# Optimization experiments

Measured on AMD Instinct MI355X. Metric: run time of the kernel, lower is better.

The kernel has to match this reference:

```python
import jax, jax.numpy as jnp
import numpy as np

B, N, DIM, QK, H, GS = 4, 4096, 512, 512, 8, 128
NUM_LABELS = 8
R_BASE, R_MIN, R_MAX = 0.5, 0.25, 0.75
LAMBDA_P, LAMBDA_V, CCR = 0.25, 0.25, 0.125


def setup_inputs() -> dict:
    key = jax.random.key(0)
    ks = jax.random.split(key, 7)
    s = DIM ** -0.5
    return {
        "x": jax.random.normal(ks[0], (B, N, DIM), jnp.float32),
        "labels": jax.random.randint(ks[1], (B, N), 0, NUM_LABELS),
        "scores": jax.random.uniform(ks[2], (B, N), jnp.float32),
        "Wq": jax.random.normal(ks[3], (DIM, QK), jnp.float32) * s,
        "Wk": jax.random.normal(ks[4], (DIM, QK), jnp.float32) * s,
        "Wv": jax.random.normal(ks[5], (DIM, DIM), jnp.float32) * s,
        "Wproj": jax.random.normal(ks[6], (DIM, DIM), jnp.float32) * s,
    }


def _windows(t, gs, ng):
    # pad with flipped last-group tail, then overlapping windows of size 2*gs, stride gs
    tp = jnp.concatenate([t, jnp.flip(t[:, -gs:], axis=1)], axis=1)
    a = tp.reshape(t.shape[0], ng + 1, gs, *t.shape[2:])
    return jnp.concatenate([a[:, :-1], a[:, 1:]], axis=2)  # [b, ng, 2*gs, ...]


def _topk_mask(vals, keep, cand):
    # rank of each entry when sorted descending; keep top-`keep` among candidates
    ranks = jnp.argsort(jnp.argsort(-vals, axis=-1), axis=-1)
    return (ranks < keep[:, :, None, None, None]) & cand


def reference(x, labels, scores, Wq, Wk, Wv, Wproj):
    b, n, _ = x.shape
    gs = GS
    ng = n // gs            # num_tokens divisible by group_size -> pad_n = 0
    ws = 2 * gs
    q = x @ Wq
    k = x @ Wk
    v = x @ Wv

    qw = q.reshape(b, ng, gs, H, -1).transpose(0, 1, 3, 2, 4)          # b ng h gs d
    kw = _windows(k, gs, ng).reshape(b, ng, ws, H, -1).transpose(0, 1, 3, 2, 4)
    vw = _windows(v, gs, ng).reshape(b, ng, ws, H, -1).transpose(0, 1, 3, 2, 4)
    q_labels = labels.reshape(b, ng, gs)
    k_labels = _windows(labels, gs, ng)                                 # b ng ws
    q_scores = scores.reshape(b, ng, gs)
    k_scores = _windows(scores, gs, ng)

    d = qw.shape[-1]
    scale = 1.0 / jnp.sqrt(jnp.asarray(d, qw.dtype))
    logits = jnp.einsum('bghqd,bghkd->bghqk', qw, kw) * scale           # b ng h gs ws
    attn_hat = jax.nn.softmax(logits, axis=-1)  # no prev_attn_state -> attn_hat = attn_cur

    # dynamic focus ratio: purity from group mode label + score variance
    counts = jax.nn.one_hot(q_labels, NUM_LABELS, dtype=jnp.float32).sum(axis=2)  # b ng L
    mode = jnp.argmax(counts, axis=-1)
    purity = jnp.mean((q_labels == mode[..., None]).astype(jnp.float32), axis=-1)
    score_var = jnp.var(q_scores.astype(jnp.float32), axis=-1)  # unbiased=False
    focus = jnp.clip(R_BASE + LAMBDA_P * purity - LAMBDA_V * score_var, R_MIN, R_MAX)

    keep = jnp.clip(jnp.ceil(focus * ws).astype(jnp.int32), 1, ws)
    cross_keep = jnp.round(keep.astype(jnp.float32) * CCR).astype(jnp.int32)
    cross_keep = jnp.where(keep > 1, jnp.maximum(cross_keep, 1), 0)
    same_keep = jnp.maximum(keep - cross_keep, 1)

    same_mask = (q_labels[:, :, None, :, None] == k_labels[:, :, None, None, :])  # b ng 1 gs ws

    same_scores = jnp.where(same_mask, attn_hat, -10000.0)
    m_same = _topk_mask(same_scores, same_keep, same_mask)
    pair_conf = q_scores[:, :, None, :, None] * k_scores[:, :, None, None, :]
    cross_scores = attn_hat * pair_conf
    m_cross = _topk_mask(cross_scores, cross_keep, ~same_mask)
    final_mask = m_same | m_cross

    sparse_logits = jnp.where(final_mask, logits, -10000.0)
    attn_local = jax.nn.softmax(sparse_logits, axis=-1)
    attn_local = jnp.where(final_mask, attn_local, 0.0)
    attn_local = attn_local / (attn_local.sum(axis=-1, keepdims=True) + 1e-9)

    out = jnp.einsum('bghqk,bghkd->bghqd', attn_local, vw)
    out = out.transpose(0, 1, 3, 2, 4).reshape(b, ng * gs, -1)[:, :n]
    return out @ Wproj, attn_local
```

## Files before the change

kernel.cpp:

```cpp
#include <hip/hip_runtime.h>

#define BB 4
#define NN 4096
#define DIMM 512
#define HH 8
#define DH 64
#define GSZ 128
#define NGRP 32
#define WSZ 256
#define CHUNK 32

#define MK 8388608u
#define WK 262144u

typedef short short8 __attribute__((ext_vector_type(8)));
typedef float f32x4 __attribute__((ext_vector_type(4)));

__device__ inline unsigned short bf16rne(float f) {
  unsigned u = __float_as_uint(f);
  unsigned r = u + 0x7FFFu + ((u >> 16) & 1u);
  return (unsigned short)(r >> 16);
}
__device__ inline float bf16tof(unsigned short h) {
  return __uint_as_float(((unsigned)h) << 16);
}

__global__ __launch_bounds__(256) void split_planes(
    const float* __restrict__ X, unsigned short* __restrict__ P)
{
  unsigned idx = (blockIdx.x * 256u + threadIdx.x) * 4u;
  float4 xv = *(const float4*)&X[idx];
  float xs[4] = {xv.x, xv.y, xv.z, xv.w};
  ushort4 hv, mv, lv;
  unsigned short* hp = (unsigned short*)&hv;
  unsigned short* mp = (unsigned short*)&mv;
  unsigned short* lp = (unsigned short*)&lv;
#pragma unroll
  for (int i = 0; i < 4; ++i) {
    unsigned short h = bf16rne(xs[i]);
    float r1 = xs[i] - bf16tof(h);
    unsigned short m = bf16rne(r1);
    float r2 = r1 - bf16tof(m);
    hp[i] = h;
    mp[i] = m;
    lp[i] = bf16rne(r2);
  }
  *(ushort4*)&P[idx] = hv;
  *(ushort4*)&P[MK + idx] = mv;
  *(ushort4*)&P[2u * MK + idx] = lv;
}

__global__ __launch_bounds__(256) void split_w(
    const float* __restrict__ Wq, const float* __restrict__ Wk,
    const float* __restrict__ Wv, const float* __restrict__ Wpj,
    unsigned short* __restrict__ wqkv, unsigned short* __restrict__ wproj)
{
  unsigned e = blockIdx.x * 256u + threadIdx.x;
  int mz = e >> 18;
  unsigned rem = e & (WK - 1u);
  unsigned kk = rem >> 9, n = rem & 511u;
  const float* src = (mz == 0) ? Wq : (mz == 1) ? Wk : (mz == 2) ? Wv : Wpj;
  float w = src[kk * 512u + n];
  unsigned short h = bf16rne(w);
  float r1 = w - bf16tof(h);
  unsigned short m = bf16rne(r1);
  float r2 = r1 - bf16tof(m);
  unsigned short l = bf16rne(r2);
  unsigned o = n * 512u + kk;
  if (mz < 3) {
    unsigned short* base = wqkv + (unsigned)mz * 3u * WK;
    base[o] = h;
    base[WK + o] = m;
    base[2u * WK + o] = l;
  } else {
    wproj[o] = h;
    wproj[WK + o] = m;
  }
}

template <int NP, int NT>
__global__ __launch_bounds__(256) void mfma_gemm(
    const unsigned short* __restrict__ Ap,
    const unsigned short* __restrict__ Wp,
    float* __restrict__ C)
{
  constexpr int ta[6] = {0, 0, 1, 1, 0, 2};
  constexpr int tw[6] = {0, 1, 0, 1, 2, 0};
  const int z = blockIdx.z;
  const int n0 = blockIdx.x * 128;
  const int m0 = blockIdx.y * 128;
  const int tid = threadIdx.x;
  const int lane = tid & 63, wv = tid >> 6;
  const int wm = (wv >> 1) * 64, wn = (wv & 1) * 64;
  const int lm = lane & 15, lk = (lane >> 4) * 8;

  __shared__ unsigned short As[NP * 128 * 40];
  __shared__ unsigned short Ws[NP * 128 * 40];

  f32x4 acc[4][4];
#pragma unroll
  for (int i = 0; i < 4; ++i)
#pragma unroll
    for (int j = 0; j < 4; ++j) acc[i][j] = (f32x4){0.f, 0.f, 0.f, 0.f};

  const unsigned short* Wz = Wp + (size_t)z * NP * WK;

  for (int k0 = 0; k0 < 512; k0 += 32) {
#pragma unroll
    for (int i = 0; i < NP * 2; ++i) {
      int idx = i * 256 + tid;
      int p = idx >> 9, rem = idx & 511;
      int r = rem >> 2, cc = rem & 3;
      *(short8*)&As[p * 5120 + r * 40 + cc * 8] =
          *(const short8*)&Ap[(size_t)p * MK + (size_t)(m0 + r) * 512 + k0 + cc * 8];
      *(short8*)&Ws[p * 5120 + r * 40 + cc * 8] =
          *(const short8*)&Wz[(size_t)p * WK + (size_t)(n0 + r) * 512 + k0 + cc * 8];
    }
    __syncthreads();

    short8 a[NP][4];
#pragma unroll
    for (int p = 0; p < NP; ++p)
#pragma unroll
      for (int fm = 0; fm < 4; ++fm)
        a[p][fm] = *(const short8*)&As[p * 5120 + (wm + fm * 16 + lm) * 40 + lk];

#pragma unroll
    for (int fn = 0; fn < 4; ++fn) {
      short8 bf[NP];
#pragma unroll
      for (int p = 0; p < NP; ++p)
        bf[p] = *(const short8*)&Ws[p * 5120 + (wn + fn * 16 + lm) * 40 + lk];
#pragma unroll
      for (int fm = 0; fm < 4; ++fm) {
#pragma unroll
        for (int t = 0; t < NT; ++t)
          acc[fm][fn] = __builtin_amdgcn_mfma_f32_16x16x32_bf16(
              a[ta[t]][fm], bf[tw[t]], acc[fm][fn], 0, 0, 0);
      }
    }
    __syncthreads();
  }

  const int rq = (lane >> 4) * 4;
  float* Cz = C + (size_t)z * 8388608u;
#pragma unroll
  for (int fm = 0; fm < 4; ++fm)
#pragma unroll
    for (int fn = 0; fn < 4; ++fn) {
      int row = m0 + wm + fm * 16 + rq;
      int col = n0 + wn + fn * 16 + lm;
#pragma unroll
      for (int r = 0; r < 4; ++r)
        Cz[(size_t)(row + r) * 512 + col] = acc[fm][fn][r];
    }
}

__global__ __launch_bounds__(256) void gemm512(
    const float* __restrict__ A,
    const float* __restrict__ W0, const float* __restrict__ W1, const float* __restrict__ W2,
    float* __restrict__ C0, float* __restrict__ C1, float* __restrict__ C2)
{
  const int z = blockIdx.z;
  const float* Wm = (z == 0) ? W0 : (z == 1 ? W1 : W2);
  float* Cm = (z == 0) ? C0 : (z == 1 ? C1 : C2);
  const int n0 = blockIdx.x * 128;
  const int m0 = blockIdx.y * 128;
  const int tid = threadIdx.x;
  const int tx = tid & 15, ty = tid >> 4;

  __shared__ float As[32][132];
  __shared__ float Bs[32][132];

  float acc[8][8];
#pragma unroll
  for (int i = 0; i < 8; ++i)
#pragma unroll
    for (int j = 0; j < 8; ++j) acc[i][j] = 0.f;

  for (int k0 = 0; k0 < 512; k0 += 32) {
    {
      const int c4 = tid & 7, r = tid >> 3;
#pragma unroll
      for (int p = 0; p < 128; p += 32) {
        float4 av = *(const float4*)&A[(size_t)(m0 + r + p) * 512 + k0 + c4 * 4];
        As[c4 * 4 + 0][r + p] = av.x;
        As[c4 * 4 + 1][r + p] = av.y;
        As[c4 * 4 + 2][r + p] = av.z;
        As[c4 * 4 + 3][r + p] = av.w;
      }
      const int j4 = tid & 31, rb = tid >> 5;
#pragma unroll
      for (int p = 0; p < 32; p += 8) {
        *(float4*)&Bs[rb + p][j4 * 4] =
            *(const float4*)&Wm[(size_t)(k0 + rb + p) * 512 + n0 + j4 * 4];
      }
    }
    __syncthreads();
#pragma unroll
    for (int kk = 0; kk < 32; ++kk) {
      float4 a0 = *(const float4*)&As[kk][ty * 8];
      float4 a1 = *(const float4*)&As[kk][ty * 8 + 4];
      float4 b0 = *(const float4*)&Bs[kk][tx * 8];
      float4 b1 = *(const float4*)&Bs[kk][tx * 8 + 4];
      float av[8] = {a0.x, a0.y, a0.z, a0.w, a1.x, a1.y, a1.z, a1.w};
      float bv[8] = {b0.x, b0.y, b0.z, b0.w, b1.x, b1.y, b1.z, b1.w};
#pragma unroll
      for (int i = 0; i < 8; ++i)
#pragma unroll
        for (int j = 0; j < 8; ++j) acc[i][j] += av[i] * bv[j];
    }
    __syncthreads();
  }
#pragma unroll
  for (int i = 0; i < 8; ++i) {
    size_t row = (size_t)(m0 + ty * 8 + i);
    float4 o0 = make_float4(acc[i][0], acc[i][1], acc[i][2], acc[i][3]);
    float4 o1 = make_float4(acc[i][4], acc[i][5], acc[i][6], acc[i][7]);
    *(float4*)&Cm[row * 512 + n0 + tx * 8] = o0;
    *(float4*)&Cm[row * 512 + n0 + tx * 8 + 4] = o1;
  }
}

__device__ __forceinline__ void focus_keep(
    const unsigned char* klab, const float* kscr, int* hist8, float* s_var,
    int* s_sk, int* s_ck, int tid, int lane, int wv)
{
  if (tid < GSZ) atomicAdd(&hist8[klab[tid]], 1);
  if (wv == 0) {
    double x0 = (double)kscr[lane], x1 = (double)kscr[lane + 64];
    double s = x0 + x1;
#pragma unroll
    for (int off = 32; off > 0; off >>= 1) s += __shfl_xor(s, off);
    double mean = s * (1.0 / 128.0);
    double d0 = x0 - mean, d1 = x1 - mean;
    double vs = d0 * d0 + d1 * d1;
#pragma unroll
    for (int off = 32; off > 0; off >>= 1) vs += __shfl_xor(vs, off);
    if (lane == 0) *s_var = (float)(vs * (1.0 / 128.0));
  }
  __syncthreads();
  if (tid == 0) {
    int bc = hist8[0];
    for (int l = 1; l < 8; ++l)
      if (hist8[l] > bc) bc = hist8[l];
    float purity = (float)bc * (1.0f / GSZ);
    float focus = 0.5f + 0.25f * purity - 0.25f * (*s_var);
    focus = fminf(fmaxf(focus, 0.25f), 0.75f);
    int keep = (int)ceilf(focus * (float)WSZ);
    keep = min(max(keep, 1), WSZ);
    int ck = keep >> 3, rem = keep & 7;
    if (rem > 4 || (rem == 4 && (ck & 1))) ck++;
    if (ck < 1) ck = 1;
    int sk = keep - ck;
    if (sk < 1) sk = 1;
    *s_sk = sk;
    *s_ck = ck;
  }
  __syncthreads();
}

__global__ __launch_bounds__(256, 3) void attn_v9(
    const float* __restrict__ q, const float* __restrict__ k,
    const float* __restrict__ vf,
    const int* __restrict__ labels, const float* __restrict__ scores,
    float* __restrict__ attn_out, unsigned short* __restrict__ opl)
{
  const int bx = blockIdx.x;
  const int c = bx >> 10;
  const int rblk = bx & 1023;
  const int h = rblk & 7;
  const int g = (rblk >> 3) & 31;
  const int b = rblk >> 8;
  const int r0 = c * CHUNK;
  const int tid = threadIdx.x;
  const int lane = tid & 63, wv = tid >> 6;
  const int lm = lane & 15, lq = lane >> 4;

  __shared__ float att[CHUNK][264];
  __shared__ __align__(16) unsigned char vbuf[18432];
  float (*ktile)[68] = (float (*)[68])vbuf;
  unsigned short* vtT = (unsigned short*)vbuf;
  __shared__ unsigned char klab[WSZ];
  __shared__ float kscr[WSZ];
  __shared__ int hist8[8];
  __shared__ float s_var;
  __shared__ int s_sk, s_ck;

  {
    int j = tid;
    int pos = g * GSZ + j;
    int tok = pos < NN ? pos : (2 * NN - 1 - pos);
    klab[j] = (unsigned char)labels[b * NN + tok];
    kscr[j] = scores[b * NN + tok];
  }
  if (tid < 8) hist8[tid] = 0;
  __syncthreads();
  focus_keep(klab, kscr, hist8, &s_var, &s_sk, &s_ck, tid, lane, wv);
  const int same_keep = s_sk, cross_keep = s_ck;

  const int rp = tid >> 4, jx = tid & 15;
  const int srow = tid >> 4, sd4 = (tid & 15) * 4;
  const float* q0p = q + (size_t)(b * NN + g * GSZ + r0 + rp) * DIMM + h * DH;
  const float* q1p = q0p + (size_t)16 * DIMM;

  for (int jt = 0; jt < 4; ++jt) {
#pragma unroll
    for (int p = 0; p < 64; p += 16) {
      int j = jt * 64 + srow + p;
      int pos = g * GSZ + j;
      int tok = pos < NN ? pos : (2 * NN - 1 - pos);
      *(float4*)&ktile[srow + p][sd4] =
          *(const float4*)&k[(size_t)(b * NN + tok) * DIMM + h * DH + sd4];
    }
    __syncthreads();
    float acc0[4] = {0.f, 0.f, 0.f, 0.f}, acc1[4] = {0.f, 0.f, 0.f, 0.f};
#pragma unroll
    for (int dd = 0; dd < DH; dd += 4) {
      float4 q0 = *(const float4*)(q0p + dd);
      float4 q1 = *(const float4*)(q1p + dd);
#pragma unroll
      for (int jj = 0; jj < 4; ++jj) {
        float4 kv = *(const float4*)&ktile[jx + 16 * jj][dd];
        acc0[jj] += q0.x * kv.x + q0.y * kv.y + q0.z * kv.z + q0.w * kv.w;
        acc1[jj] += q1.x * kv.x + q1.y * kv.y + q1.z * kv.z + q1.w * kv.w;
      }
    }
#pragma unroll
    for (int jj = 0; jj < 4; ++jj) {
      att[rp][jt * 64 + jx + 16 * jj] = acc0[jj] * 0.125f;
      att[rp + 16][jt * 64 + jx + 16 * jj] = acc1[jj] * 0.125f;
    }
    __syncthreads();
  }

  {
    int kl0[4];
    float ks0[4];
#pragma unroll
    for (int m = 0; m < 4; ++m) {
      kl0[m] = klab[lane + 64 * m];
      ks0[m] = kscr[lane + 64 * m];
    }
    for (int sp = 0; sp < 4; ++sp) {
      const int rA = wv * 8 + 2 * sp, rB = rA + 1;
      const int qLA = klab[r0 + rA], qLB = klab[r0 + rB];
      const float qSA = kscr[r0 + rA], qSB = kscr[r0 + rB];
      float aA[4], aB[4];
      float mxA = -INFINITY, mxB = -INFINITY;
#pragma unroll
      for (int m = 0; m < 4; ++m) {
        aA[m] = att[rA][lane + 64 * m];
        aB[m] = att[rB][lane + 64 * m];
        mxA = fmaxf(mxA, aA[m]);
        mxB = fmaxf(mxB, aB[m]);
      }
#pragma unroll
      for (int off = 32; off > 0; off >>= 1) {
        mxA = fmaxf(mxA, __shfl_xor(mxA, off));
        mxB = fmaxf(mxB, __shfl_xor(mxB, off));
      }
      unsigned fsA[4], fcA[4], fsB[4], fcB[4];
      bool cdA[4], cdB[4];
#pragma unroll
      for (int m = 0; m < 4; ++m) {
        aA[m] = expf(aA[m] - mxA);
        aB[m] = expf(aB[m] - mxB);
        cdA[m] = (kl0[m] == qLA);
        cdB[m] = (kl0[m] == qLB);
        fsA[m] = cdA[m] ? __float_as_uint(aA[m]) : 0u;
        fsB[m] = cdB[m] ? __float_as_uint(aB[m]) : 0u;
        fcA[m] = __float_as_uint(aA[m] * (qSA * ks0[m]));
        fcB[m] = __float_as_uint(aB[m] * (qSB * ks0[m]));
      }
      unsigned tsA = 0, tcA = 0, tsB = 0, tcB = 0;
      for (int bit = 29; bit >= 0; --bit) {
        unsigned csA = tsA | (1u << bit), ccA = tcA | (1u << bit);
        unsigned csB = tsB | (1u << bit), ccB = tcB | (1u << bit);
        int nsA = 0, ncA = 0, nsB = 0, ncB = 0;
#pragma unroll
        for (int m = 0; m < 4; ++m) {
          nsA += __popcll(__ballot(fsA[m] >= csA));
          ncA += __popcll(__ballot(fcA[m] >= ccA));
          nsB += __popcll(__ballot(fsB[m] >= csB));
          ncB += __popcll(__ballot(fcB[m] >= ccB));
        }
        if (nsA >= same_keep) tsA = csA;
        if (ncA >= cross_keep) tcA = ccA;
        if (nsB >= same_keep) tsB = csB;
        if (ncB >= cross_keep) tcB = ccB;
      }
#pragma unroll
      for (int rsel = 0; rsel < 2; ++rsel) {
        const int rr = rsel ? rB : rA;
        const unsigned ts = rsel ? tsB : tsA, tc = rsel ? tcB : tcA;
        unsigned* fs = rsel ? fsB : fsA;
        unsigned* fc = rsel ? fcB : fcA;
        float* a = rsel ? aB : aA;
        bool* cand = rsel ? cdB : cdA;
        unsigned long long beqs[4], beqc[4];
        int gts = 0, gtc = 0;
#pragma unroll
        for (int m = 0; m < 4; ++m) {
          gts += __popcll(__ballot(fs[m] > ts));
          gtc += __popcll(__ballot(fc[m] > tc));
          beqs[m] = __ballot(fs[m] == ts);
          beqc[m] = __ballot(fc[m] == tc);
        }
        const int rs = same_keep - gts, rc = cross_keep - gtc;
        float pv[4];
        float S = 0.f;
        int pres = 0, prec = 0;
#pragma unroll
        for (int m = 0; m < 4; ++m) {
          int mbs = __builtin_amdgcn_mbcnt_hi((unsigned)(beqs[m] >> 32),
                     __builtin_amdgcn_mbcnt_lo((unsigned)beqs[m], 0));
          int mbc = __builtin_amdgcn_mbcnt_hi((unsigned)(beqc[m] >> 32),
                     __builtin_amdgcn_mbcnt_lo((unsigned)beqc[m], 0));
          bool keep_s = cand[m] && ((fs[m] > ts) || ((fs[m] == ts) && (pres + mbs < rs)));
          bool keep_c = (!cand[m]) && ((fc[m] > tc) || ((fc[m] == tc) && (prec + mbc < rc)));
          pv[m] = (keep_s || keep_c) ? a[m] : 0.f;
          S += pv[m];
          pres += __popcll(beqs[m]);
          prec += __popcll(beqc[m]);
        }
#pragma unroll
        for (int off = 32; off > 0; off >>= 1) S += __shfl_xor(S, off);
        const float inv = 1.0f / S;
        size_t gb = ((((size_t)b * NGRP + g) * HH + h) * GSZ + (r0 + rr)) * WSZ + lane;
        unsigned short* prow = (unsigned short*)&att[rr][0];
#pragma unroll
        for (int m = 0; m < 4; ++m) {
          float p = pv[m] * inv;
          attn_out[gb + 64 * m] = p;
          unsigned short hh = bf16rne(p);
          prow[lane + 64 * m] = hh;
          prow[264 + lane + 64 * m] = bf16rne(p - bf16tof(hh));
        }
      }
    }
  }

  f32x4 acc2[2] = {(f32x4){0.f, 0.f, 0.f, 0.f}, (f32x4){0.f, 0.f, 0.f, 0.f}};
  for (int jt = 0; jt < 4; ++jt) {
    __syncthreads();
    {
      const int dx_ = tid & 15, jh = tid >> 4;
#pragma unroll
      for (int ps = 0; ps < 2; ++ps) {
        int jl0 = ps * 32 + 2 * jh;
        float4 v0, v1;
#pragma unroll
        for (int qq = 0; qq < 2; ++qq) {
          int pos = g * GSZ + jt * 64 + jl0 + qq;
          int tok = pos < NN ? pos : (2 * NN - 1 - pos);
          float4 vv = *(const float4*)&vf[(size_t)(b * NN + tok) * DIMM + h * DH + dx_ * 4];
          if (qq == 0) v0 = vv; else v1 = vv;
        }
        const float* a0 = (const float*)&v0;
        const float* a1 = (const float*)&v1;
#pragma unroll
        for (int i = 0; i < 4; ++i) {
          int d = dx_ * 4 + i;
          unsigned short h0 = bf16rne(a0[i]);
          unsigned short h1 = bf16rne(a1[i]);
          unsigned short m0 = bf16rne(a0[i] - bf16tof(h0));
          unsigned short m1 = bf16rne(a1[i] - bf16tof(h1));
          *(unsigned*)&vtT[0 * 4608 + d * 72 + jl0] = (unsigned)h0 | ((unsigned)h1 << 16);
          *(unsigned*)&vtT[1 * 4608 + d * 72 + jl0] = (unsigned)m0 | ((unsigned)m1 << 16);
        }
      }
    }
    __syncthreads();
#pragma unroll
    for (int kt = 0; kt < 2; ++kt) {
      const int koff = jt * 64 + kt * 32 + lq * 8;
      short8 ahi[2], ami[2];
#pragma unroll
      for (int mt = 0; mt < 2; ++mt) {
        const unsigned short* arow = (const unsigned short*)&att[mt * 16 + lm][0];
        ahi[mt] = *(const short8*)&arow[koff];
        ami[mt] = *(const short8*)&arow[264 + koff];
      }
      const int vo = (wv * 16 + lm) * 72 + kt * 32 + lq * 8;
      short8 bhi = *(const short8*)&vtT[vo];
      short8 bmi = *(const short8*)&vtT[4608 + vo];
#pragma unroll
      for (int mt = 0; mt < 2; ++mt) {
        acc2[mt] = __builtin_amdgcn_mfma_f32_16x16x32_bf16(ahi[mt], bhi, acc2[mt], 0, 0, 0);
        acc2[mt] = __builtin_amdgcn_mfma_f32_16x16x32_bf16(ahi[mt], bmi, acc2[mt], 0, 0, 0);
        acc2[mt] = __builtin_amdgcn_mfma_f32_16x16x32_bf16(ami[mt], bhi, acc2[mt], 0, 0, 0);
      }
    }
  }

  {
    size_t rowbase = (size_t)(b * NN + g * GSZ + r0);
#pragma unroll
    for (int mt = 0; mt < 2; ++mt)
#pragma unroll
      for (int r = 0; r < 4; ++r) {
        int row = mt * 16 + lq * 4 + r;
        float val = acc2[mt][r];
        unsigned short hh = bf16rne(val);
        size_t oaddr = (rowbase + row) * 512 + h * 64 + wv * 16 + lm;
        opl[oaddr] = hh;
        opl[MK + oaddr] = bf16rne(val - bf16tof(hh));
      }
  }
}

__global__ __launch_bounds__(256, 3) void attn_f32(
    const float* q, const float* __restrict__ k, const float* __restrict__ v,
    const int* __restrict__ labels, const float* __restrict__ scores,
    float* __restrict__ attn_out, float* o)
{
  const int bx = blockIdx.x;
  const int c = bx >> 10;
  const int rblk = bx & 1023;
  const int h = rblk & 7;
  const int g = (rblk >> 3) & 31;
  const int b = rblk >> 8;
  const int r0 = c * CHUNK;
  const int tid = threadIdx.x;
  const int lane = tid & 63, wv = tid >> 6;

  __shared__ float att[CHUNK][WSZ + 4];
  __shared__ float ktile[64][DH + 4];
  __shared__ unsigned char klab[WSZ];
  __shared__ float kscr[WSZ];
  __shared__ int hist8[8];
  __shared__ float s_var;
  __shared__ int s_sk, s_ck;

  {
    int j = tid;
    int pos = g * GSZ + j;
    int tok = pos < NN ? pos : (2 * NN - 1 - pos);
    klab[j] = (unsigned char)labels[b * NN + tok];
    kscr[j] = scores[b * NN + tok];
  }
  if (tid < 8) hist8[tid] = 0;
  __syncthreads();
  focus_keep(klab, kscr, hist8, &s_var, &s_sk, &s_ck, tid, lane, wv);
  const int same_keep = s_sk, cross_keep = s_ck;

  const int rp = tid >> 4, jx = tid & 15;
  const int srow = tid >> 4, sd4 = (tid & 15) * 4;
  const float* q0p = q + (size_t)(b * NN + g * GSZ + r0 + rp) * DIMM + h * DH;
  const float* q1p = q0p + (size_t)16 * DIMM;

  for (int jt = 0; jt < 4; ++jt) {
#pragma unroll
    for (int p = 0; p < 64; p += 16) {
      int j = jt * 64 + srow + p;
      int pos = g * GSZ + j;
      int tok = pos < NN ? pos : (2 * NN - 1 - pos);
      *(float4*)&ktile[srow + p][sd4] =
          *(const float4*)&k[(size_t)(b * NN + tok) * DIMM + h * DH + sd4];
    }
    __syncthreads();
    float acc0[4] = {0.f, 0.f, 0.f, 0.f}, acc1[4] = {0.f, 0.f, 0.f, 0.f};
#pragma unroll
    for (int dd = 0; dd < DH; dd += 4) {
      float4 q0 = *(const float4*)(q0p + dd);
      float4 q1 = *(const float4*)(q1p + dd);
#pragma unroll
      for (int jj = 0; jj < 4; ++jj) {
        float4 kv = *(const float4*)&ktile[jx + 16 * jj][dd];
        acc0[jj] += q0.x * kv.x + q0.y * kv.y + q0.z * kv.z + q0.w * kv.w;
        acc1[jj] += q1.x * kv.x + q1.y * kv.y + q1.z * kv.z + q1.w * kv.w;
      }
    }
#pragma unroll
    for (int jj = 0; jj < 4; ++jj) {
      att[rp][jt * 64 + jx + 16 * jj] = acc0[jj] * 0.125f;
      att[rp + 16][jt * 64 + jx + 16 * jj] = acc1[jj] * 0.125f;
    }
    __syncthreads();
  }

  {
    int kl0[4];
    float ks0[4];
#pragma unroll
    for (int m = 0; m < 4; ++m) {
      kl0[m] = klab[lane + 64 * m];
      ks0[m] = kscr[lane + 64 * m];
    }
    for (int sp = 0; sp < 4; ++sp) {
      const int rA = wv * 8 + 2 * sp, rB = rA + 1;
      const int qLA = klab[r0 + rA], qLB = klab[r0 + rB];
      const float qSA = kscr[r0 + rA], qSB = kscr[r0 + rB];
      float aA[4], aB[4];
      float mxA = -INFINITY, mxB = -INFINITY;
#pragma unroll
      for (int m = 0; m < 4; ++m) {
        aA[m] = att[rA][lane + 64 * m];
        aB[m] = att[rB][lane + 64 * m];
        mxA = fmaxf(mxA, aA[m]);
        mxB = fmaxf(mxB, aB[m]);
      }
#pragma unroll
      for (int off = 32; off > 0; off >>= 1) {
        mxA = fmaxf(mxA, __shfl_xor(mxA, off));
        mxB = fmaxf(mxB, __shfl_xor(mxB, off));
      }
      unsigned fsA[4], fcA[4], fsB[4], fcB[4];
      bool cdA[4], cdB[4];
#pragma unroll
      for (int m = 0; m < 4; ++m) {
        aA[m] = expf(aA[m] - mxA);
        aB[m] = expf(aB[m] - mxB);
        cdA[m] = (kl0[m] == qLA);
        cdB[m] = (kl0[m] == qLB);
        fsA[m] = cdA[m] ? __float_as_uint(aA[m]) : 0u;
        fsB[m] = cdB[m] ? __float_as_uint(aB[m]) : 0u;
        fcA[m] = __float_as_uint(aA[m] * (qSA * ks0[m]));
        fcB[m] = __float_as_uint(aB[m] * (qSB * ks0[m]));
      }
      unsigned tsA = 0, tcA = 0, tsB = 0, tcB = 0;
      for (int bit = 29; bit >= 0; --bit) {
        unsigned csA = tsA | (1u << bit), ccA = tcA | (1u << bit);
        unsigned csB = tsB | (1u << bit), ccB = tcB | (1u << bit);
        int nsA = 0, ncA = 0, nsB = 0, ncB = 0;
#pragma unroll
        for (int m = 0; m < 4; ++m) {
          nsA += __popcll(__ballot(fsA[m] >= csA));
          ncA += __popcll(__ballot(fcA[m] >= ccA));
          nsB += __popcll(__ballot(fsB[m] >= csB));
          ncB += __popcll(__ballot(fcB[m] >= ccB));
        }
        if (nsA >= same_keep) tsA = csA;
        if (ncA >= cross_keep) tcA = ccA;
        if (nsB >= same_keep) tsB = csB;
        if (ncB >= cross_keep) tcB = ccB;
      }
#pragma unroll
      for (int rsel = 0; rsel < 2; ++rsel) {
        const int rr = rsel ? rB : rA;
        const unsigned ts = rsel ? tsB : tsA, tc = rsel ? tcB : tcA;
        unsigned* fs = rsel ? fsB : fsA;
        unsigned* fc = rsel ? fcB : fcA;
        float* a = rsel ? aB : aA;
        bool* cand = rsel ? cdB : cdA;
        unsigned long long beqs[4], beqc[4];
        int gts = 0, gtc = 0;
#pragma unroll
        for (int m = 0; m < 4; ++m) {
          gts += __popcll(__ballot(fs[m] > ts));
          gtc += __popcll(__ballot(fc[m] > tc));
          beqs[m] = __ballot(fs[m] == ts);
          beqc[m] = __ballot(fc[m] == tc);
        }
        const int rs = same_keep - gts, rc = cross_keep - gtc;
        float pv[4];
        float S = 0.f;
        int pres = 0, prec = 0;
#pragma unroll
        for (int m = 0; m < 4; ++m) {
          int mbs = __builtin_amdgcn_mbcnt_hi((unsigned)(beqs[m] >> 32),
                     __builtin_amdgcn_mbcnt_lo((unsigned)beqs[m], 0));
          int mbc = __builtin_amdgcn_mbcnt_hi((unsigned)(beqc[m] >> 32),
                     __builtin_amdgcn_mbcnt_lo((unsigned)beqc[m], 0));
          bool keep_s = cand[m] && ((fs[m] > ts) || ((fs[m] == ts) && (pres + mbs < rs)));
          bool keep_c = (!cand[m]) && ((fc[m] > tc) || ((fc[m] == tc) && (prec + mbc < rc)));
          pv[m] = (keep_s || keep_c) ? a[m] : 0.f;
          S += pv[m];
          pres += __popcll(beqs[m]);
          prec += __popcll(beqc[m]);
        }
#pragma unroll
        for (int off = 32; off > 0; off >>= 1) S += __shfl_xor(S, off);
        const float inv = 1.0f / S;
        size_t gb = ((((size_t)b * NGRP + g) * HH + h) * GSZ + (r0 + rr)) * WSZ + lane;
#pragma unroll
        for (int m = 0; m < 4; ++m) {
          float p = pv[m] * inv;
          att[rr][lane + 64 * m] = p;
          attn_out[gb + 64 * m] = p;
        }
      }
    }
  }
  __syncthreads();

  const int dx = jx;
  float oa0[4] = {0.f, 0.f, 0.f, 0.f}, oa1[4] = {0.f, 0.f, 0.f, 0.f};
  for (int jt = 0; jt < 4; ++jt) {
#pragma unroll
    for (int p = 0; p < 64; p += 16) {
      int j = jt * 64 + srow + p;
      int pos = g * GSZ + j;
      int tok = pos < NN ? pos : (2 * NN - 1 - pos);
      *(float4*)&ktile[srow + p][sd4] =
          *(const float4*)&v[(size_t)(b * NN + tok) * DIMM + h * DH + sd4];
    }
    __syncthreads();
#pragma unroll 4
    for (int jg = 0; jg < 16; ++jg) {
      float4 p0 = *(const float4*)&att[rp][jt * 64 + jg * 4];
      float4 p1 = *(const float4*)&att[rp + 16][jt * 64 + jg * 4];
      float4 v0 = *(const float4*)&ktile[jg * 4 + 0][dx * 4];
      float4 v1 = *(const float4*)&ktile[jg * 4 + 1][dx * 4];
      float4 v2 = *(const float4*)&ktile[jg * 4 + 2][dx * 4];
      float4 v3 = *(const float4*)&ktile[jg * 4 + 3][dx * 4];
      oa0[0] += p0.x * v0.x + p0.y * v1.x + p0.z * v2.x + p0.w * v3.x;
      oa0[1] += p0.x * v0.y + p0.y * v1.y + p0.z * v2.y + p0.w * v3.y;
      oa0[2] += p0.x * v0.z + p0.y * v1.z + p0.z * v2.z + p0.w * v3.z;
      oa0[3] += p0.x * v0.w + p0.y * v1.w + p0.z * v2.w + p0.w * v3.w;
      oa1[0] += p1.x * v0.x + p1.y * v1.x + p1.z * v2.x + p1.w * v3.x;
      oa1[1] += p1.x * v0.y + p1.y * v1.y + p1.z * v2.y + p1.w * v3.y;
      oa1[2] += p1.x * v0.z + p1.y * v1.z + p1.z * v2.z + p1.w * v3.z;
      oa1[3] += p1.x * v0.w + p1.y * v1.w + p1.z * v2.w + p1.w * v3.w;
    }
    __syncthreads();
  }
  {
    size_t ob0 = (size_t)(b * NN + g * GSZ + r0 + rp) * DIMM + h * DH + dx * 4;
    *(float4*)&o[ob0] = make_float4(oa0[0], oa0[1], oa0[2], oa0[3]);
    *(float4*)&o[ob0 + (size_t)16 * DIMM] = make_float4(oa1[0], oa1[1], oa1[2], oa1[3]);
  }
}

extern "C" void kernel_launch(void* const* d_in, const int* in_sizes, int n_in,
                              void* d_out, int out_size, void* d_ws, size_t ws_size,
                              hipStream_t stream) {
  const float* x      = (const float*)d_in[0];
  const int*   labels = (const int*)d_in[1];
  const float* scores = (const float*)d_in[2];
  const float* Wq     = (const float*)d_in[3];
  const float* Wk     = (const float*)d_in[4];
  const float* Wv     = (const float*)d_in[5];
  const float* Wproj  = (const float*)d_in[6];

  float* out = (float*)d_out;
  float* attn_out = out + (size_t)BB * NN * DIMM;

  float* qb = (float*)d_ws;
  float* kb = qb + (size_t)MK;
  float* vf = kb + (size_t)MK;
  unsigned short* xpl  = (unsigned short*)(vf + (size_t)MK);
  unsigned short* wqkv = xpl + 3 * (size_t)MK;
  unsigned short* wpp  = wqkv + 9 * (size_t)WK;
  const size_t required = 3 * (size_t)MK * 4 + 3 * (size_t)MK * 2 + 11 * (size_t)WK * 2;

  if (ws_size >= required) {
    split_planes<<<dim3(MK / 1024), 256, 0, stream>>>(x, xpl);
    split_w<<<dim3(4 * WK / 256), 256, 0, stream>>>(Wq, Wk, Wv, Wproj, wqkv, wpp);
    mfma_gemm<3, 6><<<dim3(4, 128, 2), 256, 0, stream>>>(xpl, wqkv, qb);
    mfma_gemm<2, 3><<<dim3(4, 128, 1), 256, 0, stream>>>(xpl, wqkv + 6 * (size_t)WK, vf);
    attn_v9<<<dim3(BB * NGRP * HH * 4), 256, 0, stream>>>(
        qb, kb, vf, labels, scores, attn_out, xpl);
    mfma_gemm<2, 3><<<dim3(4, 128, 1), 256, 0, stream>>>(xpl, wpp, out);
  } else {
    const size_t SZ = (size_t)BB * NN * DIMM;
    float* q2 = (float*)d_ws;
    float* k2 = q2 + SZ;
    float* v2 = k2 + SZ;
    gemm512<<<dim3(4, 128, 3), 256, 0, stream>>>(x, Wq, Wk, Wv, q2, k2, v2);
    attn_f32<<<dim3(BB * NGRP * HH * 4), 256, 0, stream>>>(
        q2, k2, v2, labels, scores, attn_out, q2);
    gemm512<<<dim3(4, 128, 1), 256, 0, stream>>>(q2, Wproj, Wproj, Wproj, out, out, out);
  }
}
```

Measured before the change: 747.6 us.

## Process attention chunk in two 16-row halves to cut LDS and raise occupancy

The attention kernel now handles its 32-row chunk as two sequential 16-row halves, halving the shared-memory score buffer and the MFMA accumulator registers, and raises launch bounds from 3 to 4 blocks per CU. The goal is more resident blocks per CU to hide latency in the serial top-k radix selection. In exchange, K tiles are loaded twice and V tiles are reloaded and re-split into bf16 planes twice per block, which adds global traffic and extra barriers.

```diff
diff --git a/kernel.cpp b/kernel.cpp
--- a/kernel.cpp
+++ b/kernel.cpp
@@ -260,7 +260,7 @@
   __syncthreads();
 }
 
-__global__ __launch_bounds__(256, 3) void attn_v9(
+__global__ __launch_bounds__(256, 4) void attn_v10(
     const float* __restrict__ q, const float* __restrict__ k,
     const float* __restrict__ vf,
     const int* __restrict__ labels, const float* __restrict__ scores,
@@ -277,7 +277,7 @@
   const int lane = tid & 63, wv = tid >> 6;
   const int lm = lane & 15, lq = lane >> 4;
 
-  __shared__ float att[CHUNK][264];
+  __shared__ float att[16][264];
   __shared__ __align__(16) unsigned char vbuf[18432];
   float (*ktile)[68] = (float (*)[68])vbuf;
   unsigned short* vtT = (unsigned short*)vbuf;
@@ -299,214 +299,212 @@
   focus_keep(klab, kscr, hist8, &s_var, &s_sk, &s_ck, tid, lane, wv);
   const int same_keep = s_sk, cross_keep = s_ck;
 
-  const int rp = tid >> 4, jx = tid & 15;
   const int srow = tid >> 4, sd4 = (tid & 15) * 4;
-  const float* q0p = q + (size_t)(b * NN + g * GSZ + r0 + rp) * DIMM + h * DH;
-  const float* q1p = q0p + (size_t)16 * DIMM;
-
-  for (int jt = 0; jt < 4; ++jt) {
-#pragma unroll
-    for (int p = 0; p < 64; p += 16) {
-      int j = jt * 64 + srow + p;
-      int pos = g * GSZ + j;
-      int tok = pos < NN ? pos : (2 * NN - 1 - pos);
-      *(float4*)&ktile[srow + p][sd4] =
-          *(const float4*)&k[(size_t)(b * NN + tok) * DIMM + h * DH + sd4];
-    }
-    __syncthreads();
-    float acc0[4] = {0.f, 0.f, 0.f, 0.f}, acc1[4] = {0.f, 0.f, 0.f, 0.f};
-#pragma unroll
-    for (int dd = 0; dd < DH; dd += 4) {
-      float4 q0 = *(const float4*)(q0p + dd);
-      float4 q1 = *(const float4*)(q1p + dd);
-#pragma unroll
-      for (int jj = 0; jj < 4; ++jj) {
-        float4 kv = *(const float4*)&ktile[jx + 16 * jj][dd];
-        acc0[jj] += q0.x * kv.x + q0.y * kv.y + q0.z * kv.z + q0.w * kv.w;
-        acc1[jj] += q1.x * kv.x + q1.y * kv.y + q1.z * kv.z + q1.w * kv.w;
-      }
-    }
-#pragma unroll
-    for (int jj = 0; jj < 4; ++jj) {
-      att[rp][jt * 64 + jx + 16 * jj] = acc0[jj] * 0.125f;
-      att[rp + 16][jt * 64 + jx + 16 * jj] = acc1[jj] * 0.125f;
-    }
-    __syncthreads();
-  }
-
-  {
-    int kl0[4];
-    float ks0[4];
-#pragma unroll
-    for (int m = 0; m < 4; ++m) {
-      kl0[m] = klab[lane + 64 * m];
-      ks0[m] = kscr[lane + 64 * m];
-    }
-    for (int sp = 0; sp < 4; ++sp) {
-      const int rA = wv * 8 + 2 * sp, rB = rA + 1;
-      const int qLA = klab[r0 + rA], qLB = klab[r0 + rB];
-      const float qSA = kscr[r0 + rA], qSB = kscr[r0 + rB];
-      float aA[4], aB[4];
-      float mxA = -INFINITY, mxB = -INFINITY;
-#pragma unroll
-      for (int m = 0; m < 4; ++m) {
-        aA[m] = att[rA][lane + 64 * m];
-        aB[m] = att[rB][lane + 64 * m];
-        mxA = fmaxf(mxA, aA[m]);
-        mxB = fmaxf(mxB, aB[m]);
-      }
-#pragma unroll
-      for (int off = 32; off > 0; off >>= 1) {
-        mxA = fmaxf(mxA, __shfl_xor(mxA, off));
-        mxB = fmaxf(mxB, __shfl_xor(mxB, off));
-      }
-      unsigned fsA[4], fcA[4], fsB[4], fcB[4];
-      bool cdA[4], cdB[4];
-#pragma unroll
-      for (int m = 0; m < 4; ++m) {
-        aA[m] = expf(aA[m] - mxA);
-        aB[m] = expf(aB[m] - mxB);
-        cdA[m] = (kl0[m] == qLA);
-        cdB[m] = (kl0[m] == qLB);
-        fsA[m] = cdA[m] ? __float_as_uint(aA[m]) : 0u;
-        fsB[m] = cdB[m] ? __float_as_uint(aB[m]) : 0u;
-        fcA[m] = __float_as_uint(aA[m] * (qSA * ks0[m]));
-        fcB[m] = __float_as_uint(aB[m] * (qSB * ks0[m]));
-      }
-      unsigned tsA = 0, tcA = 0, tsB = 0, tcB = 0;
-      for (int bit = 29; bit >= 0; --bit) {
-        unsigned csA = tsA | (1u << bit), ccA = tcA | (1u << bit);
-        unsigned csB = tsB | (1u << bit), ccB = tcB | (1u << bit);
-        int nsA = 0, ncA = 0, nsB = 0, ncB = 0;
+  const int rp2 = tid >> 5, jx2 = tid & 31;
+
+  int kl0[4];
+  float ks0[4];
+#pragma unroll
+  for (int m = 0; m < 4; ++m) {
+    kl0[m] = klab[lane + 64 * m];
+    ks0[m] = kscr[lane + 64 * m];
+  }
+
+  for (int half = 0; half < 2; ++half) {
+    const int rbase = r0 + half * 16;
+    __syncthreads();
+
+    const float* q0p = q + (size_t)(b * NN + g * GSZ + rbase + rp2) * DIMM + h * DH;
+    const float* q1p = q0p + (size_t)8 * DIMM;
+
+    for (int jt = 0; jt < 4; ++jt) {
+#pragma unroll
+      for (int p = 0; p < 64; p += 16) {
+        int j = jt * 64 + srow + p;
+        int pos = g * GSZ + j;
+        int tok = pos < NN ? pos : (2 * NN - 1 - pos);
+        *(float4*)&ktile[srow + p][sd4] =
+            *(const float4*)&k[(size_t)(b * NN + tok) * DIMM + h * DH + sd4];
+      }
+      __syncthreads();
+      float acc0[2] = {0.f, 0.f}, acc1[2] = {0.f, 0.f};
+#pragma unroll
+      for (int dd = 0; dd < DH; dd += 4) {
+        float4 q0 = *(const float4*)(q0p + dd);
+        float4 q1 = *(const float4*)(q1p + dd);
+#pragma unroll
+        for (int jj = 0; jj < 2; ++jj) {
+          float4 kv = *(const float4*)&ktile[jx2 + 32 * jj][dd];
+          acc0[jj] += q0.x * kv.x + q0.y * kv.y + q0.z * kv.z + q0.w * kv.w;
+          acc1[jj] += q1.x * kv.x + q1.y * kv.y + q1.z * kv.z + q1.w * kv.w;
+        }
+      }
+#pragma unroll
+      for (int jj = 0; jj < 2; ++jj) {
+        att[rp2][jt * 64 + jx2 + 32 * jj] = acc0[jj] * 0.125f;
+        att[rp2 + 8][jt * 64 + jx2 + 32 * jj] = acc1[jj] * 0.125f;
+      }
+      __syncthreads();
+    }
+
+    {
+      for (int sp = 0; sp < 2; ++sp) {
+        const int rA = wv * 4 + 2 * sp, rB = rA + 1;
+        const int qLA = klab[rbase + rA], qLB = klab[rbase + rB];
+        const float qSA = kscr[rbase + rA], qSB = kscr[rbase + rB];
+        float aA[4], aB[4];
+        float mxA = -INFINITY, mxB = -INFINITY;
 #pragma unroll
         for (int m = 0; m < 4; ++m) {
-          nsA += __popcll(__ballot(fsA[m] >= csA));
-          ncA += __popcll(__ballot(fcA[m] >= ccA));
-          nsB += __popcll(__ballot(fsB[m] >= csB));
-          ncB += __popcll(__ballot(fcB[m] >= ccB));
-        }
-        if (nsA >= same_keep) tsA = csA;
-        if (ncA >= cross_keep) tcA = ccA;
-        if (nsB >= same_keep) tsB = csB;
-        if (ncB >= cross_keep) tcB = ccB;
-      }
-#pragma unroll
-      for (int rsel = 0; rsel < 2; ++rsel) {
-        const int rr = rsel ? rB : rA;
-        const unsigned ts = rsel ? tsB : tsA, tc = rsel ? tcB : tcA;
-        unsigned* fs = rsel ? fsB : fsA;
-        unsigned* fc = rsel ? fcB : fcA;
-        float* a = rsel ? aB : aA;
-        bool* cand = rsel ? cdB : cdA;
-        unsigned long long beqs[4], beqc[4];
-        int gts = 0, gtc = 0;
+          aA[m] = att[rA][lane + 64 * m];
+          aB[m] = att[rB][lane + 64 * m];
+          mxA = fmaxf(mxA, aA[m]);
+          mxB = fmaxf(mxB, aB[m]);
+        }
+#pragma unroll
+        for (int off = 32; off > 0; off >>= 1) {
+          mxA = fmaxf(mxA, __shfl_xor(mxA, off));
+          mxB = fmaxf(mxB, __shfl_xor(mxB, off));
+        }
+        unsigned fsA[4], fcA[4], fsB[4], fcB[4];
+        bool cdA[4], cdB[4];
 #pragma unroll
         for (int m = 0; m < 4; ++m) {
-          gts += __popcll(__ballot(fs[m] > ts));
-          gtc += __popcll(__ballot(fc[m] > tc));
-          beqs[m] = __ballot(fs[m] == ts);
-          beqc[m] = __ballot(fc[m] == tc);
-        }
-        const int rs = same_keep - gts, rc = cross_keep - gtc;
-        float pv[4];
-        float S = 0.f;
-        int pres = 0, prec = 0;
-#pragma unroll
-        for (int m = 0; m < 4; ++m) {
-          int mbs = __builtin_amdgcn_mbcnt_hi((unsigned)(beqs[m] >> 32),
-                     __builtin_amdgcn_mbcnt_lo((unsigned)beqs[m], 0));
-          int mbc = __builtin_amdgcn_mbcnt_hi((unsigned)(beqc[m] >> 32),
-                     __builtin_amdgcn_mbcnt_lo((unsigned)beqc[m], 0));
-          bool keep_s = cand[m] && ((fs[m] > ts) || ((fs[m] == ts) && (pres + mbs < rs)));
-          bool keep_c = (!cand[m]) && ((fc[m] > tc) || ((fc[m] == tc) && (prec + mbc < rc)));
-          pv[m] = (keep_s || keep_c) ? a[m] : 0.f;
-          S += pv[m];
-          pres += __popcll(beqs[m]);
-          prec += __popcll(beqc[m]);
-        }
-#pragma unroll
-        for (int off = 32; off > 0; off >>= 1) S += __shfl_xor(S, off);
-        const float inv = 1.0f / S;
-        size_t gb = ((((size_t)b * NGRP + g) * HH + h) * GSZ + (r0 + rr)) * WSZ + lane;
-        unsigned short* prow = (unsigned short*)&att[rr][0];
-#pragma unroll
-        for (int m = 0; m < 4; ++m) {
-          float p = pv[m] * inv;
-          attn_out[gb + 64 * m] = p;
-          unsigned short hh = bf16rne(p);
-          prow[lane + 64 * m] = hh;
-          prow[264 + lane + 64 * m] = bf16rne(p - bf16tof(hh));
-        }
-      }
-    }
-  }
-
-  f32x4 acc2[2] = {(f32x4){0.f, 0.f, 0.f, 0.f}, (f32x4){0.f, 0.f, 0.f, 0.f}};
-  for (int jt = 0; jt < 4; ++jt) {
-    __syncthreads();
+          aA[m] = expf(aA[m] - mxA);
+          aB[m] = expf(aB[m] - mxB);
+          cdA[m] = (kl0[m] == qLA);
+          cdB[m] = (kl0[m] == qLB);
+          fsA[m] = cdA[m] ? __float_as_uint(aA[m]) : 0u;
+          fsB[m] = cdB[m] ? __float_as_uint(aB[m]) : 0u;
+          fcA[m] = __float_as_uint(aA[m] * (qSA * ks0[m]));
+          fcB[m] = __float_as_uint(aB[m] * (qSB * ks0[m]));
+        }
+        unsigned tsA = 0, tcA = 0, tsB = 0, tcB = 0;
+        for (int bit = 29; bit >= 0; --bit) {
+          unsigned csA = tsA | (1u << bit), ccA = tcA | (1u << bit);
+          unsigned csB = tsB | (1u << bit), ccB = tcB | (1u << bit);
+          int nsA = 0, ncA = 0, nsB = 0, ncB = 0;
+#pragma unroll
+          for (int m = 0; m < 4; ++m) {
+            nsA += __popcll(__ballot(fsA[m] >= csA));
+            ncA += __popcll(__ballot(fcA[m] >= ccA));
+            nsB += __popcll(__ballot(fsB[m] >= csB));
+            ncB += __popcll(__ballot(fcB[m] >= ccB));
+          }
+          if (nsA >= same_keep) tsA = csA;
+          if (ncA >= cross_keep) tcA = ccA;
+          if (nsB >= same_keep) tsB = csB;
+          if (ncB >= cross_keep) tcB = ccB;
+        }
+#pragma unroll
+        for (int rsel = 0; rsel < 2; ++rsel) {
+          const int rr = rsel ? rB : rA;
+          const unsigned ts = rsel ? tsB : tsA, tc = rsel ? tcB : tcA;
+          unsigned* fs = rsel ? fsB : fsA;
+          unsigned* fc = rsel ? fcB : fcA;
+          float* a = rsel ? aB : aA;
+          bool* cand = rsel ? cdB : cdA;
+          unsigned long long beqs[4], beqc[4];
+          int gts = 0, gtc = 0;
+#pragma unroll
+          for (int m = 0; m < 4; ++m) {
+            gts += __popcll(__ballot(fs[m] > ts));
+            gtc += __popcll(__ballot(fc[m] > tc));
+            beqs[m] = __ballot(fs[m] == ts);
+            beqc[m] = __ballot(fc[m] == tc);
+          }
+          const int rs = same_keep - gts, rc = cross_keep - gtc;
+          float pv[4];
+          float S = 0.f;
+          int pres = 0, prec = 0;
+#pragma unroll
+          for (int m = 0; m < 4; ++m) {
+            int mbs = __builtin_amdgcn_mbcnt_hi((unsigned)(beqs[m] >> 32),
+                       __builtin_amdgcn_mbcnt_lo((unsigned)beqs[m], 0));
+            int mbc = __builtin_amdgcn_mbcnt_hi((unsigned)(beqc[m] >> 32),
+                       __builtin_amdgcn_mbcnt_lo((unsigned)beqc[m], 0));
+            bool keep_s = cand[m] && ((fs[m] > ts) || ((fs[m] == ts) && (pres + mbs < rs)));
+            bool keep_c = (!cand[m]) && ((fc[m] > tc) || ((fc[m] == tc) && (prec + mbc < rc)));
+            pv[m] = (keep_s || keep_c) ? a[m] : 0.f;
+            S += pv[m];
+            pres += __popcll(beqs[m]);
+            prec += __popcll(beqc[m]);
+          }
+#pragma unroll
+          for (int off = 32; off > 0; off >>= 1) S += __shfl_xor(S, off);
+          const float inv = 1.0f / S;
+          size_t gb = ((((size_t)b * NGRP + g) * HH + h) * GSZ + (rbase + rr)) * WSZ + lane;
+          unsigned short* prow = (unsigned short*)&att[rr][0];
+#pragma unroll
+          for (int m = 0; m < 4; ++m) {
+            float p = pv[m] * inv;
+            attn_out[gb + 64 * m] = p;
+            unsigned short hh = bf16rne(p);
+            prow[lane + 64 * m] = hh;
+            prow[264 + lane + 64 * m] = bf16rne(p - bf16tof(hh));
+          }
+        }
+      }
+    }
+
+    f32x4 acc2 = (f32x4){0.f, 0.f, 0.f, 0.f};
+    for (int jt = 0; jt < 4; ++jt) {
+      __syncthreads();
+      {
+        const int dx_ = tid & 15, jh = tid >> 4;
+#pragma unroll
+        for (int ps = 0; ps < 2; ++ps) {
+          int jl0 = ps * 32 + 2 * jh;
+          float4 v0, v1;
+#pragma unroll
+          for (int qq = 0; qq < 2; ++qq) {
+            int pos = g * GSZ + jt * 64 + jl0 + qq;
+            int tok = pos < NN ? pos : (2 * NN - 1 - pos);
+            float4 vv = *(const float4*)&vf[(size_t)(b * NN + tok) * DIMM + h * DH + dx_ * 4];
+            if (qq == 0) v0 = vv; else v1 = vv;
+          }
+          const float* a0 = (const float*)&v0;
+          const float* a1 = (const float*)&v1;
+#pragma unroll
+          for (int i = 0; i < 4; ++i) {
+            int d = dx_ * 4 + i;
+            unsigned short h0 = bf16rne(a0[i]);
+            unsigned short h1 = bf16rne(a1[i]);
+            unsigned short m0 = bf16rne(a0[i] - bf16tof(h0));
+            unsigned short m1 = bf16rne(a1[i] - bf16tof(h1));
+            *(unsigned*)&vtT[0 * 4608 + d * 72 + jl0] = (unsigned)h0 | ((unsigned)h1 << 16);
+            *(unsigned*)&vtT[1 * 4608 + d * 72 + jl0] = (unsigned)m0 | ((unsigned)m1 << 16);
+          }
+        }
+      }
+      __syncthreads();
+#pragma unroll
+      for (int kt = 0; kt < 2; ++kt) {
+        const int koff = jt * 64 + kt * 32 + lq * 8;
+        const unsigned short* arow = (const unsigned short*)&att[lm][0];
+        short8 ahi = *(const short8*)&arow[koff];
+        short8 ami = *(const short8*)&arow[264 + koff];
+        const int vo = (wv * 16 + lm) * 72 + kt * 32 + lq * 8;
+        short8 bhi = *(const short8*)&vtT[vo];
+        short8 bmi = *(const short8*)&vtT[4608 + vo];
+        acc2 = __builtin_amdgcn_mfma_f32_16x16x32_bf16(ahi, bhi, acc2, 0, 0, 0);
+        acc2 = __builtin_amdgcn_mfma_f32_16x16x32_bf16(ahi, bmi, acc2, 0, 0, 0);
+        acc2 = __builtin_amdgcn_mfma_f32_16x16x32_bf16(ami, bhi, acc2, 0, 0, 0);
+      }
+    }
+
     {
-      const int dx_ = tid & 15, jh = tid >> 4;
-#pragma unroll
-      for (int ps = 0; ps < 2; ++ps) {
-        int jl0 = ps * 32 + 2 * jh;
-        float4 v0, v1;
-#pragma unroll
-        for (int qq = 0; qq < 2; ++qq) {
-          int pos = g * GSZ + jt * 64 + jl0 + qq;
-          int tok = pos < NN ? pos : (2 * NN - 1 - pos);
-          float4 vv = *(const float4*)&vf[(size_t)(b * NN + tok) * DIMM + h * DH + dx_ * 4];
-          if (qq == 0) v0 = vv; else v1 = vv;
-        }
-        const float* a0 = (const float*)&v0;
-        const float* a1 = (const float*)&v1;
-#pragma unroll
-        for (int i = 0; i < 4; ++i) {
-          int d = dx_ * 4 + i;
-          unsigned short h0 = bf16rne(a0[i]);
-          unsigned short h1 = bf16rne(a1[i]);
-          unsigned short m0 = bf16rne(a0[i] - bf16tof(h0));
-          unsigned short m1 = bf16rne(a1[i] - bf16tof(h1));
-          *(unsigned*)&vtT[0 * 4608 + d * 72 + jl0] = (unsigned)h0 | ((unsigned)h1 << 16);
-          *(unsigned*)&vtT[1 * 4608 + d * 72 + jl0] = (unsigned)m0 | ((unsigned)m1 << 16);
-        }
-      }
-    }
-    __syncthreads();
-#pragma unroll
-    for (int kt = 0; kt < 2; ++kt) {
-      const int koff = jt * 64 + kt * 32 + lq * 8;
-      short8 ahi[2], ami[2];
-#pragma unroll
-      for (int mt = 0; mt < 2; ++mt) {
-        const unsigned short* arow = (const unsigned short*)&att[mt * 16 + lm][0];
-        ahi[mt] = *(const short8*)&arow[koff];
-        ami[mt] = *(const short8*)&arow[264 + koff];
-      }
-      const int vo = (wv * 16 + lm) * 72 + kt * 32 + lq * 8;
-      short8 bhi = *(const short8*)&vtT[vo];
-      short8 bmi = *(const short8*)&vtT[4608 + vo];
-#pragma unroll
-      for (int mt = 0; mt < 2; ++mt) {
-        acc2[mt] = __builtin_amdgcn_mfma_f32_16x16x32_bf16(ahi[mt], bhi, acc2[mt], 0, 0, 0);
-        acc2[mt] = __builtin_amdgcn_mfma_f32_16x16x32_bf16(ahi[mt], bmi, acc2[mt], 0, 0, 0);
-        acc2[mt] = __builtin_amdgcn_mfma_f32_16x16x32_bf16(ami[mt], bhi, acc2[mt], 0, 0, 0);
-      }
-    }
-  }
-
-  {
-    size_t rowbase = (size_t)(b * NN + g * GSZ + r0);
-#pragma unroll
-    for (int mt = 0; mt < 2; ++mt)
+      size_t rowbase = (size_t)(b * NN + g * GSZ + rbase);
 #pragma unroll
       for (int r = 0; r < 4; ++r) {
-        int row = mt * 16 + lq * 4 + r;
-        float val = acc2[mt][r];
+        int row = lq * 4 + r;
+        float val = acc2[r];
         unsigned short hh = bf16rne(val);
         size_t oaddr = (rowbase + row) * 512 + h * 64 + wv * 16 + lm;
         opl[oaddr] = hh;
         opl[MK + oaddr] = bf16rne(val - bf16tof(hh));
       }
+    }
   }
 }
 
@@ -750,7 +748,7 @@
     split_w<<<dim3(4 * WK / 256), 256, 0, stream>>>(Wq, Wk, Wv, Wproj, wqkv, wpp);
     mfma_gemm<3, 6><<<dim3(4, 128, 2), 256, 0, stream>>>(xpl, wqkv, qb);
     mfma_gemm<2, 3><<<dim3(4, 128, 1), 256, 0, stream>>>(xpl, wqkv + 6 * (size_t)WK, vf);
-    attn_v9<<<dim3(BB * NGRP * HH * 4), 256, 0, stream>>>(
+    attn_v10<<<dim3(BB * NGRP * HH * 4), 256, 0, stream>>>(
         qb, kb, vf, labels, scores, attn_out, xpl);
     mfma_gemm<2, 3><<<dim3(4, 128, 1), 256, 0, stream>>>(xpl, wpp, out);
   } else {
```

After: 888.4 us. 1.19x slower.
